# Performance work log

Measured on AMD Instinct MI355X. Metric: run time of the kernel, lower is better.

The kernel has to match this reference:

```python
import jax, jax.numpy as jnp
import numpy as np

N_NODES = 50000


def gcn_conv(x, src, dst, W, b, num_nodes):
    """PyG GCNConv: y = D^{-1/2} (A + I) D^{-1/2} (x @ W) + b.
    src/dst already include self-loops."""
    h = x @ W  # [N, F_out]
    deg = jax.ops.segment_sum(jnp.ones_like(dst, dtype=h.dtype), dst,
                              num_segments=num_nodes)  # in-degree incl. self-loop
    dinv = jnp.where(deg > 0, jax.lax.rsqrt(deg), 0.0)
    norm = dinv[src] * dinv[dst]  # [E]
    msgs = h[src] * norm[:, None]  # gather + scale, [E, F_out]
    out = jax.ops.segment_sum(msgs, dst, num_segments=num_nodes)
    return out + b


def setup_inputs() -> dict:
    key = jax.random.key(0)
    k1, k2, k3, k4 = jax.random.split(key, 4)
    latent, hidden, out_ch = 64, 128, 64
    n_edges = 800000
    z = jax.random.normal(k1, (N_NODES, latent), dtype=jnp.float32)
    edge_index = jax.random.randint(k2, (2, n_edges), 0, N_NODES, dtype=jnp.int64)
    # Glorot-style scaled weights
    W1 = jax.random.normal(k3, (latent, hidden), dtype=jnp.float32) * (1.0 / np.sqrt(latent))
    b1 = jnp.zeros((hidden,), dtype=jnp.float32)
    W2 = jax.random.normal(k4, (hidden, out_ch), dtype=jnp.float32) * (1.0 / np.sqrt(hidden))
    b2 = jnp.zeros((out_ch,), dtype=jnp.float32)
    return {"z": z, "edge_index": edge_index, "W1": W1, "b1": b1, "W2": W2, "b2": b2}


def reference(z, edge_index, W1, b1, W2, b2):
    num_nodes = z.shape[0]
    loops = jnp.arange(num_nodes, dtype=edge_index.dtype)
    src = jnp.concatenate([edge_index[0], loops])  # add self-loops
    dst = jnp.concatenate([edge_index[1], loops])
    x = gcn_conv(z, src, dst, W1, b1, num_nodes)
    x = jax.nn.relu(x)
    x = gcn_conv(x, src, dst, W2, b2, num_nodes)
    x = jax.nn.relu(x)
    return x
```

## Files before the change

### kernel.cpp

```cpp
#include <hip/hip_runtime.h>
#include <hip/hip_fp16.h>

static inline size_t align256(size_t x){ return (x + 255) & ~(size_t)255; }

#define CAP 64
#define NPART 8

__device__ __forceinline__ int detect_is64(const unsigned* __restrict__ e){
  unsigned v = e[2 * (threadIdx.x & 63) + 1];
  return (__ballot(v != 0u) == 0ull) ? 1 : 0;
}

__device__ __forceinline__ int load_idx(const void* edges, long i, int is64){
  return is64 ? (int)((const long long*)edges)[i] : ((const int*)edges)[i];
}

__global__ __launch_bounds__(256) void pack_kernel(const void* __restrict__ edges, int E,
                                                   unsigned* __restrict__ pe,
                                                   int* __restrict__ cnt, int N){
  const int is64 = detect_is64((const unsigned*)edges);
  const int t0 = blockIdx.x * 256 + threadIdx.x;
  const int stride = gridDim.x * 256;
  for (int i = t0; i < N; i += stride) cnt[i] = 0;
  for (int i = t0; i < E; i += stride){
    const unsigned s = (unsigned)load_idx(edges, i, is64);
    const unsigned d = (unsigned)load_idx(edges, (long)E + i, is64);
    pe[i] = (d << 16) | (s & 0xFFFFu);
  }
}

__global__ __launch_bounds__(256) void build_kernel(const unsigned* __restrict__ pe, int E,
                                                    int* __restrict__ cnt,
                                                    unsigned short* __restrict__ csr,
                                                    int N){
  const int p  = blockIdx.x & (NPART - 1);
  const int q  = blockIdx.x >> 3;
  const int nq = gridDim.x >> 3;
  const int nper = (N + NPART - 1) / NPART;
  const int lo = p * nper;
  const int hi = min(lo + nper, N);
  const int stride = nq * 256;
  for (int i = q * 256 + threadIdx.x; i < E; i += stride){
    const unsigned v = pe[i];
    const int d = (int)(v >> 16);
    if (d < lo || d >= hi) continue;
    const int pos = atomicAdd(&cnt[d], 1);
    if (pos < CAP) csr[((size_t)d << 6) + pos] = (unsigned short)(v & 0xFFFFu);
  }
}

__device__ __forceinline__ void h8_acc(uint4 r, float* a){
  const __half2* h = (const __half2*)&r;
  #pragma unroll
  for (int k = 0; k < 4; ++k){
    const float2 f = __half22float2(h[k]);
    a[2*k]     += f.x;
    a[2*k + 1] += f.y;
  }
}

__device__ __forceinline__ void gather8(const uint4* __restrict__ H,
                                        const unsigned short* __restrict__ row,
                                        int deg, int j, float* a){
  int e = 0;
  #pragma unroll 1
  for (; e + 4 <= deg; e += 4){
    const ushort4 rr = *(const ushort4*)(row + e);
    const uint4 v0 = H[(size_t)rr.x * 8 + j];
    const uint4 v1 = H[(size_t)rr.y * 8 + j];
    const uint4 v2 = H[(size_t)rr.z * 8 + j];
    const uint4 v3 = H[(size_t)rr.w * 8 + j];
    h8_acc(v0, a); h8_acc(v1, a); h8_acc(v2, a); h8_acc(v3, a);
  }
  #pragma unroll 1
  for (; e < deg; ++e) h8_acc(H[(size_t)row[e] * 8 + j], a);
}

__global__ __launch_bounds__(256) void prep_kernel(const float4* __restrict__ z,
                                                   uint4* __restrict__ zh,
                                                   const int* __restrict__ cnt,
                                                   float* __restrict__ dinv, int N){
  const int idx = blockIdx.x * 256 + threadIdx.x;
  const int node = idx >> 3;
  if (node >= N) return;
  const int j = idx & 7;
  const float di = rsqrtf((float)(cnt[node] + 1));
  if (j == 0) dinv[node] = di;
  const float4 v0 = z[(size_t)node * 16 + j * 2];
  const float4 v1 = z[(size_t)node * 16 + j * 2 + 1];
  const __half2 a0 = __float22half2_rn(make_float2(di * v0.x, di * v0.y));
  const __half2 a1 = __float22half2_rn(make_float2(di * v0.z, di * v0.w));
  const __half2 a2 = __float22half2_rn(make_float2(di * v1.x, di * v1.y));
  const __half2 a3 = __float22half2_rn(make_float2(di * v1.z, di * v1.w));
  uint4 r;
  r.x = *(const unsigned*)&a0; r.y = *(const unsigned*)&a1;
  r.z = *(const unsigned*)&a2; r.w = *(const unsigned*)&a3;
  zh[idx] = r;
}

#define X1LD 132
__global__ __launch_bounds__(512) void fused1_kernel(const uint4* __restrict__ zh,
                                                     const unsigned short* __restrict__ csr,
                                                     const int* __restrict__ cnt,
                                                     const float* __restrict__ dinv,
                                                     const float* __restrict__ W1,
                                                     const float* __restrict__ b1,
                                                     const float* __restrict__ W2,
                                                     __half* __restrict__ h2, int N){
  __shared__ unsigned short wl[64 * 128];
  __shared__ float rows[64 * 64];
  __shared__ unsigned short x1t[64 * X1LD];
  const int t = threadIdx.x;

  {
    const float4* Wg = (const float4*)W1;
    #pragma unroll
    for (int c = 0; c < 4; ++c){
      const int gi = t + c * 512;
      const float4 v = Wg[gi];
      const __half2 h0 = __float22half2_rn(make_float2(v.x, v.y));
      const __half2 h1 = __float22half2_rn(make_float2(v.z, v.w));
      uint2 r; r.x = *(const unsigned*)&h0; r.y = *(const unsigned*)&h1;
      *(uint2*)&wl[gi * 4] = r;
    }
  }

  const int local = t >> 3;
  const int j = t & 7;
  const int node = blockIdx.x * 64 + local;
  float a[8] = {0.f, 0.f, 0.f, 0.f, 0.f, 0.f, 0.f, 0.f};
  if (node < N){
    h8_acc(zh[(size_t)node * 8 + j], a);
    const int deg = min(cnt[node], CAP);
    gather8(zh, csr + ((size_t)node << 6), deg, j, a);
    const float di = dinv[node];
    #pragma unroll
    for (int k = 0; k < 8; ++k) a[k] *= di;
  }
  float4* rp = (float4*)&rows[t * 8];
  rp[0] = make_float4(a[0], a[1], a[2], a[3]);
  rp[1] = make_float4(a[4], a[5], a[6], a[7]);
  __syncthreads();

  const int jc = t & 127;
  const int g = t >> 7;
  {
    const float bv = b1[jc];
    float accv[16];
    #pragma unroll
    for (int n = 0; n < 16; ++n) accv[n] = bv;

    #pragma unroll 2
    for (int k4 = 0; k4 < 16; ++k4){
      const float w0 = __half2float(*(const __half*)&wl[(4 * k4 + 0) * 128 + jc]);
      const float w1 = __half2float(*(const __half*)&wl[(4 * k4 + 1) * 128 + jc]);
      const float w2 = __half2float(*(const __half*)&wl[(4 * k4 + 2) * 128 + jc]);
      const float w3 = __half2float(*(const __half*)&wl[(4 * k4 + 3) * 128 + jc]);
      #pragma unroll
      for (int n = 0; n < 16; ++n){
        const float4 r = ((const float4*)rows)[(g * 16 + n) * 16 + k4];
        accv[n] = fmaf(r.x, w0, accv[n]);
        accv[n] = fmaf(r.y, w1, accv[n]);
        accv[n] = fmaf(r.z, w2, accv[n]);
        accv[n] = fmaf(r.w, w3, accv[n]);
      }
    }
    #pragma unroll
    for (int n = 0; n < 16; ++n){
      const __half hv = __float2half(fmaxf(accv[n], 0.0f));
      x1t[(g * 16 + n) * X1LD + jc] = *(const unsigned short*)&hv;
    }
  }
  __syncthreads();

  {
    const float4* Wg = (const float4*)W2;
    #pragma unroll
    for (int c = 0; c < 4; ++c){
      const int gi = t + c * 512;
      const float4 v = Wg[gi];
      const __half2 h0 = __float22half2_rn(make_float2(v.x, v.y));
      const __half2 h1 = __float22half2_rn(make_float2(v.z, v.w));
      uint2 r; r.x = *(const unsigned*)&h0; r.y = *(const unsigned*)&h1;
      *(uint2*)&wl[gi * 4] = r;
    }
  }
  __syncthreads();

  const int cg = t & 15;
  const int ng = t >> 4;
  const int n0 = ng * 2, n1 = n0 + 1;
  float acc0[4] = {0.f,0.f,0.f,0.f}, acc1[4] = {0.f,0.f,0.f,0.f};
  #pragma unroll 4
  for (int k4 = 0; k4 < 32; ++k4){
    const int k = k4 * 4;
    const uint2 xa = *(const uint2*)&x1t[n0 * X1LD + k];
    const uint2 xb = *(const uint2*)&x1t[n1 * X1LD + k];
    float xf0[4], xf1[4];
    {
      const float2 p0 = __half22float2(*(const __half2*)&xa.x);
      const float2 p1 = __half22float2(*(const __half2*)&xa.y);
      xf0[0]=p0.x; xf0[1]=p0.y; xf0[2]=p1.x; xf0[3]=p1.y;
      const float2 q0 = __half22float2(*(const __half2*)&xb.x);
      const float2 q1 = __half22float2(*(const __half2*)&xb.y);
      xf1[0]=q0.x; xf1[1]=q0.y; xf1[2]=q1.x; xf1[3]=q1.y;
    }
    #pragma unroll
    for (int dk = 0; dk < 4; ++dk){
      const uint2 wv = *(const uint2*)&wl[(k + dk) * 64 + cg * 4];
      const float2 w01 = __half22float2(*(const __half2*)&wv.x);
      const float2 w23 = __half22float2(*(const __half2*)&wv.y);
      acc0[0] = fmaf(xf0[dk], w01.x, acc0[0]);
      acc0[1] = fmaf(xf0[dk], w01.y, acc0[1]);
      acc0[2] = fmaf(xf0[dk], w23.x, acc0[2]);
      acc0[3] = fmaf(xf0[dk], w23.y, acc0[3]);
      acc1[0] = fmaf(xf1[dk], w01.x, acc1[0]);
      acc1[1] = fmaf(xf1[dk], w01.y, acc1[1]);
      acc1[2] = fmaf(xf1[dk], w23.x, acc1[2]);
      acc1[3] = fmaf(xf1[dk], w23.y, acc1[3]);
    }
  }
  const int gn0 = blockIdx.x * 64 + n0;
  const int gn1 = gn0 + 1;
  if (gn0 < N){
    const float d0 = dinv[gn0];
    const __half2 h0 = __float22half2_rn(make_float2(acc0[0]*d0, acc0[1]*d0));
    const __half2 h1 = __float22half2_rn(make_float2(acc0[2]*d0, acc0[3]*d0));
    uint2 r; r.x = *(const unsigned*)&h0; r.y = *(const unsigned*)&h1;
    *(uint2*)&h2[(size_t)gn0 * 64 + cg * 4] = r;
  }
  if (gn1 < N){
    const float d1 = dinv[gn1];
    const __half2 h0 = __float22half2_rn(make_float2(acc1[0]*d1, acc1[1]*d1));
    const __half2 h1 = __float22half2_rn(make_float2(acc1[2]*d1, acc1[3]*d1));
    uint2 r; r.x = *(const unsigned*)&h0; r.y = *(const unsigned*)&h1;
    *(uint2*)&h2[(size_t)gn1 * 64 + cg * 4] = r;
  }
}

__global__ __launch_bounds__(256) void agg2_kernel(const uint4* __restrict__ X,
                                                   float4* __restrict__ Y,
                                                   const unsigned short* __restrict__ csr,
                                                   const int* __restrict__ cnt,
                                                   const float* __restrict__ dinv,
                                                   const float4* __restrict__ bias,
                                                   int N){
  const int local = threadIdx.x >> 3;
  const int j = threadIdx.x & 7;
  const int node = blockIdx.x * 32 + local;
  if (node >= N) return;
  float a[8] = {0.f, 0.f, 0.f, 0.f, 0.f, 0.f, 0.f, 0.f};
  h8_acc(X[(size_t)node * 8 + j], a);
  const int deg = min(cnt[node], CAP);
  gather8(X, csr + ((size_t)node << 6), deg, j, a);
  const float di = dinv[node];
  const float4 b0 = bias[j * 2];
  const float4 b1v = bias[j * 2 + 1];
  float4 o0, o1;
  o0.x = fmaxf(fmaf(di, a[0], b0.x), 0.f);
  o0.y = fmaxf(fmaf(di, a[1], b0.y), 0.f);
  o0.z = fmaxf(fmaf(di, a[2], b0.z), 0.f);
  o0.w = fmaxf(fmaf(di, a[3], b0.w), 0.f);
  o1.x = fmaxf(fmaf(di, a[4], b1v.x), 0.f);
  o1.y = fmaxf(fmaf(di, a[5], b1v.y), 0.f);
  o1.z = fmaxf(fmaf(di, a[6], b1v.z), 0.f);
  o1.w = fmaxf(fmaf(di, a[7], b1v.w), 0.f);
  Y[(size_t)node * 16 + j * 2] = o0;
  Y[(size_t)node * 16 + j * 2 + 1] = o1;
}

extern "C" void kernel_launch(void* const* d_in, const int* in_sizes, int n_in,
                              void* d_out, int out_size, void* d_ws, size_t ws_size,
                              hipStream_t stream){
  const float* z  = (const float*)d_in[0];
  const void*  edges = d_in[1];
  const float* W1 = (const float*)d_in[2];
  const float* b1 = (const float*)d_in[3];
  const float* W2 = (const float*)d_in[4];
  const float* b2 = (const float*)d_in[5];
  float* out = (float*)d_out;

  constexpr int F0 = 64;
  const int N = in_sizes[0] / F0;
  const int E = in_sizes[1] / 2;
  (void)n_in; (void)out_size;

  char* p = (char*)d_ws;
  int*            cnt  = (int*)p;            p += align256((size_t)N * 4);
  float*          dinv = (float*)p;          p += align256((size_t)N * 4);
  unsigned short* csr  = (unsigned short*)p; p += align256((size_t)N * CAP * 2);
  unsigned*       pe   = (unsigned*)p;       p += align256((size_t)E * 4);
  __half*         zh   = (__half*)p;         p += align256((size_t)N * F0 * 2);
  __half*         h2   = (__half*)p;         p += align256((size_t)N * F0 * 2);
  (void)ws_size;

  pack_kernel<<<1024, 256, 0, stream>>>(edges, E, pe, cnt, N);
  build_kernel<<<1024, 256, 0, stream>>>(pe, E, cnt, csr, N);
  prep_kernel<<<(N * 8 + 255) / 256, 256, 0, stream>>>(
      (const float4*)z, (uint4*)zh, cnt, dinv, N);

  fused1_kernel<<<(N + 63) / 64, 512, 0, stream>>>(
      (const uint4*)zh, csr, cnt, dinv, W1, b1, W2, h2, N);

  agg2_kernel<<<(N + 31) / 32, 256, 0, stream>>>(
      (const uint4*)h2, (float4*)out, csr, cnt, dinv, (const float4*)b2, N);
}
```

Baseline: 196.3 us.

## Split feature tables into two planes and map blocks to XCD node partitions

Stores the fp16 feature tables as two 32-feature planes, so each gather pass touches a half-width, more cache-resident table. The layer-2 aggregation becomes two launches, one per plane, and layer-1 gathers both planes in sequence. Block indices are remapped so that blocks with the same index mod 8 handle one contiguous node partition, which aims to keep each XCD's L2 working set local. The cost is twice as many gather passes over the CSR rows and an extra kernel launch.

```diff
diff --git a/kernel.cpp b/kernel.cpp
--- a/kernel.cpp
+++ b/kernel.cpp
@@ -10,7 +10,6 @@
   unsigned v = e[2 * (threadIdx.x & 63) + 1];
   return (__ballot(v != 0u) == 0ull) ? 1 : 0;
 }
-
 __device__ __forceinline__ int load_idx(const void* edges, long i, int is64){
   return is64 ? (int)((const long long*)edges)[i] : ((const int*)edges)[i];
 }
@@ -49,68 +48,70 @@
   }
 }
 
-__device__ __forceinline__ void h8_acc(uint4 r, float* a){
-  const __half2* h = (const __half2*)&r;
-  #pragma unroll
-  for (int k = 0; k < 4; ++k){
-    const float2 f = __half22float2(h[k]);
-    a[2*k]     += f.x;
-    a[2*k + 1] += f.y;
-  }
-}
-
-__device__ __forceinline__ void gather8(const uint4* __restrict__ H,
+__device__ __forceinline__ void h4_acc(uint2 r, float* a){
+  const float2 f0 = __half22float2(*(const __half2*)&r.x);
+  const float2 f1 = __half22float2(*(const __half2*)&r.y);
+  a[0] += f0.x; a[1] += f0.y; a[2] += f1.x; a[3] += f1.y;
+}
+
+__device__ __forceinline__ void gather4(const uint2* __restrict__ P,
                                         const unsigned short* __restrict__ row,
                                         int deg, int j, float* a){
   int e = 0;
   #pragma unroll 1
-  for (; e + 4 <= deg; e += 4){
-    const ushort4 rr = *(const ushort4*)(row + e);
-    const uint4 v0 = H[(size_t)rr.x * 8 + j];
-    const uint4 v1 = H[(size_t)rr.y * 8 + j];
-    const uint4 v2 = H[(size_t)rr.z * 8 + j];
-    const uint4 v3 = H[(size_t)rr.w * 8 + j];
-    h8_acc(v0, a); h8_acc(v1, a); h8_acc(v2, a); h8_acc(v3, a);
+  for (; e + 8 <= deg; e += 8){
+    const ushort4 r0 = *(const ushort4*)(row + e);
+    const ushort4 r1 = *(const ushort4*)(row + e + 4);
+    const uint2 v0 = P[(size_t)r0.x * 8 + j];
+    const uint2 v1 = P[(size_t)r0.y * 8 + j];
+    const uint2 v2 = P[(size_t)r0.z * 8 + j];
+    const uint2 v3 = P[(size_t)r0.w * 8 + j];
+    const uint2 v4 = P[(size_t)r1.x * 8 + j];
+    const uint2 v5 = P[(size_t)r1.y * 8 + j];
+    const uint2 v6 = P[(size_t)r1.z * 8 + j];
+    const uint2 v7 = P[(size_t)r1.w * 8 + j];
+    h4_acc(v0, a); h4_acc(v1, a); h4_acc(v2, a); h4_acc(v3, a);
+    h4_acc(v4, a); h4_acc(v5, a); h4_acc(v6, a); h4_acc(v7, a);
   }
   #pragma unroll 1
-  for (; e < deg; ++e) h8_acc(H[(size_t)row[e] * 8 + j], a);
+  for (; e < deg; ++e) h4_acc(P[(size_t)row[e] * 8 + j], a);
 }
 
 __global__ __launch_bounds__(256) void prep_kernel(const float4* __restrict__ z,
-                                                   uint4* __restrict__ zh,
+                                                   uint2* __restrict__ zh,
                                                    const int* __restrict__ cnt,
                                                    float* __restrict__ dinv, int N){
   const int idx = blockIdx.x * 256 + threadIdx.x;
-  const int node = idx >> 3;
+  const int node = idx >> 4;
   if (node >= N) return;
-  const int j = idx & 7;
+  const int sub = idx & 15;
+  const int pl = sub >> 3;
+  const int j = sub & 7;
   const float di = rsqrtf((float)(cnt[node] + 1));
-  if (j == 0) dinv[node] = di;
-  const float4 v0 = z[(size_t)node * 16 + j * 2];
-  const float4 v1 = z[(size_t)node * 16 + j * 2 + 1];
-  const __half2 a0 = __float22half2_rn(make_float2(di * v0.x, di * v0.y));
-  const __half2 a1 = __float22half2_rn(make_float2(di * v0.z, di * v0.w));
-  const __half2 a2 = __float22half2_rn(make_float2(di * v1.x, di * v1.y));
-  const __half2 a3 = __float22half2_rn(make_float2(di * v1.z, di * v1.w));
-  uint4 r;
-  r.x = *(const unsigned*)&a0; r.y = *(const unsigned*)&a1;
-  r.z = *(const unsigned*)&a2; r.w = *(const unsigned*)&a3;
-  zh[idx] = r;
+  if (sub == 0) dinv[node] = di;
+  const float4 v = z[(size_t)node * 16 + pl * 8 + j];
+  const __half2 h0 = __float22half2_rn(make_float2(di * v.x, di * v.y));
+  const __half2 h1 = __float22half2_rn(make_float2(di * v.z, di * v.w));
+  uint2 r; r.x = *(const unsigned*)&h0; r.y = *(const unsigned*)&h1;
+  zh[((size_t)pl * N + node) * 8 + j] = r;
 }
 
 #define X1LD 132
-__global__ __launch_bounds__(512) void fused1_kernel(const uint4* __restrict__ zh,
+__global__ __launch_bounds__(512) void fused1_kernel(const uint2* __restrict__ zh,
                                                      const unsigned short* __restrict__ csr,
                                                      const int* __restrict__ cnt,
                                                      const float* __restrict__ dinv,
                                                      const float* __restrict__ W1,
                                                      const float* __restrict__ b1,
                                                      const float* __restrict__ W2,
-                                                     __half* __restrict__ h2, int N){
+                                                     uint2* __restrict__ h2,
+                                                     int N, int NPER){
   __shared__ unsigned short wl[64 * 128];
   __shared__ float rows[64 * 64];
   __shared__ unsigned short x1t[64 * X1LD];
   const int t = threadIdx.x;
+  const int p = blockIdx.x & (NPART - 1);
+  const int q = blockIdx.x >> 3;
 
   {
     const float4* Wg = (const float4*)W1;
@@ -127,19 +128,27 @@
 
   const int local = t >> 3;
   const int j = t & 7;
-  const int node = blockIdx.x * 64 + local;
-  float a[8] = {0.f, 0.f, 0.f, 0.f, 0.f, 0.f, 0.f, 0.f};
-  if (node < N){
-    h8_acc(zh[(size_t)node * 8 + j], a);
-    const int deg = min(cnt[node], CAP);
-    gather8(zh, csr + ((size_t)node << 6), deg, j, a);
-    const float di = dinv[node];
-    #pragma unroll
-    for (int k = 0; k < 8; ++k) a[k] *= di;
-  }
-  float4* rp = (float4*)&rows[t * 8];
-  rp[0] = make_float4(a[0], a[1], a[2], a[3]);
-  rp[1] = make_float4(a[4], a[5], a[6], a[7]);
+  const int ln = q * 64 + local;
+  const int node = p * NPER + ln;
+  const bool valid = (ln < NPER) && (node < N);
+  float di = 0.f; int deg = 0;
+  const unsigned short* row = csr;
+  if (valid){
+    di = dinv[node];
+    deg = min(cnt[node], CAP);
+    row = csr + ((size_t)node << 6);
+  }
+  #pragma unroll
+  for (int pl = 0; pl < 2; ++pl){
+    float a[4] = {0.f, 0.f, 0.f, 0.f};
+    if (valid){
+      const uint2* P = zh + (size_t)pl * N * 8;
+      h4_acc(P[(size_t)node * 8 + j], a);
+      gather4(P, row, deg, j, a);
+    }
+    *(float4*)&rows[local * 64 + pl * 32 + j * 4] =
+        make_float4(a[0] * di, a[1] * di, a[2] * di, a[3] * di);
+  }
   __syncthreads();
 
   const int jc = t & 127;
@@ -220,53 +229,56 @@
       acc1[3] = fmaf(xf1[dk], w23.y, acc1[3]);
     }
   }
-  const int gn0 = blockIdx.x * 64 + n0;
-  const int gn1 = gn0 + 1;
-  if (gn0 < N){
+  const int pl = cg >> 3;
+  const int u2 = cg & 7;
+  const int ln0 = q * 64 + n0;
+  const int gn0 = p * NPER + ln0;
+  if (ln0 < NPER && gn0 < N){
     const float d0 = dinv[gn0];
     const __half2 h0 = __float22half2_rn(make_float2(acc0[0]*d0, acc0[1]*d0));
     const __half2 h1 = __float22half2_rn(make_float2(acc0[2]*d0, acc0[3]*d0));
     uint2 r; r.x = *(const unsigned*)&h0; r.y = *(const unsigned*)&h1;
-    *(uint2*)&h2[(size_t)gn0 * 64 + cg * 4] = r;
-  }
-  if (gn1 < N){
+    h2[((size_t)pl * N + gn0) * 8 + u2] = r;
+  }
+  const int ln1 = ln0 + 1;
+  const int gn1 = gn0 + 1;
+  if (ln1 < NPER && gn1 < N){
     const float d1 = dinv[gn1];
     const __half2 h0 = __float22half2_rn(make_float2(acc1[0]*d1, acc1[1]*d1));
     const __half2 h1 = __float22half2_rn(make_float2(acc1[2]*d1, acc1[3]*d1));
     uint2 r; r.x = *(const unsigned*)&h0; r.y = *(const unsigned*)&h1;
-    *(uint2*)&h2[(size_t)gn1 * 64 + cg * 4] = r;
-  }
-}
-
-__global__ __launch_bounds__(256) void agg2_kernel(const uint4* __restrict__ X,
+    h2[((size_t)pl * N + gn1) * 8 + u2] = r;
+  }
+}
+
+template<int PL>
+__global__ __launch_bounds__(256) void agg2_kernel(const uint2* __restrict__ h2,
                                                    float4* __restrict__ Y,
                                                    const unsigned short* __restrict__ csr,
                                                    const int* __restrict__ cnt,
                                                    const float* __restrict__ dinv,
                                                    const float4* __restrict__ bias,
-                                                   int N){
+                                                   int N, int NPER){
+  const int p = blockIdx.x & (NPART - 1);
+  const int q = blockIdx.x >> 3;
   const int local = threadIdx.x >> 3;
   const int j = threadIdx.x & 7;
-  const int node = blockIdx.x * 32 + local;
-  if (node >= N) return;
-  float a[8] = {0.f, 0.f, 0.f, 0.f, 0.f, 0.f, 0.f, 0.f};
-  h8_acc(X[(size_t)node * 8 + j], a);
+  const int ln = q * 32 + local;
+  const int node = p * NPER + ln;
+  if (ln >= NPER || node >= N) return;
+  const uint2* P = h2 + (size_t)PL * N * 8;
+  float a[4] = {0.f, 0.f, 0.f, 0.f};
+  h4_acc(P[(size_t)node * 8 + j], a);
   const int deg = min(cnt[node], CAP);
-  gather8(X, csr + ((size_t)node << 6), deg, j, a);
+  gather4(P, csr + ((size_t)node << 6), deg, j, a);
   const float di = dinv[node];
-  const float4 b0 = bias[j * 2];
-  const float4 b1v = bias[j * 2 + 1];
-  float4 o0, o1;
-  o0.x = fmaxf(fmaf(di, a[0], b0.x), 0.f);
-  o0.y = fmaxf(fmaf(di, a[1], b0.y), 0.f);
-  o0.z = fmaxf(fmaf(di, a[2], b0.z), 0.f);
-  o0.w = fmaxf(fmaf(di, a[3], b0.w), 0.f);
-  o1.x = fmaxf(fmaf(di, a[4], b1v.x), 0.f);
-  o1.y = fmaxf(fmaf(di, a[5], b1v.y), 0.f);
-  o1.z = fmaxf(fmaf(di, a[6], b1v.z), 0.f);
-  o1.w = fmaxf(fmaf(di, a[7], b1v.w), 0.f);
-  Y[(size_t)node * 16 + j * 2] = o0;
-  Y[(size_t)node * 16 + j * 2 + 1] = o1;
+  const float4 b = bias[PL * 8 + j];
+  float4 o;
+  o.x = fmaxf(fmaf(di, a[0], b.x), 0.f);
+  o.y = fmaxf(fmaf(di, a[1], b.y), 0.f);
+  o.z = fmaxf(fmaf(di, a[2], b.z), 0.f);
+  o.w = fmaxf(fmaf(di, a[3], b.w), 0.f);
+  Y[(size_t)node * 16 + PL * 8 + j] = o;
 }
 
 extern "C" void kernel_launch(void* const* d_in, const int* in_sizes, int n_in,
@@ -283,6 +295,7 @@
   constexpr int F0 = 64;
   const int N = in_sizes[0] / F0;
   const int E = in_sizes[1] / 2;
+  const int NPER = (N + NPART - 1) / NPART;
   (void)n_in; (void)out_size;
 
   char* p = (char*)d_ws;
@@ -290,18 +303,22 @@
   float*          dinv = (float*)p;          p += align256((size_t)N * 4);
   unsigned short* csr  = (unsigned short*)p; p += align256((size_t)N * CAP * 2);
   unsigned*       pe   = (unsigned*)p;       p += align256((size_t)E * 4);
-  __half*         zh   = (__half*)p;         p += align256((size_t)N * F0 * 2);
-  __half*         h2   = (__half*)p;         p += align256((size_t)N * F0 * 2);
+  uint2*          zh   = (uint2*)p;          p += align256((size_t)N * 16 * 8);
+  uint2*          h2   = (uint2*)p;          p += align256((size_t)N * 16 * 8);
   (void)ws_size;
 
   pack_kernel<<<1024, 256, 0, stream>>>(edges, E, pe, cnt, N);
   build_kernel<<<1024, 256, 0, stream>>>(pe, E, cnt, csr, N);
-  prep_kernel<<<(N * 8 + 255) / 256, 256, 0, stream>>>(
-      (const float4*)z, (uint4*)zh, cnt, dinv, N);
-
-  fused1_kernel<<<(N + 63) / 64, 512, 0, stream>>>(
-      (const uint4*)zh, csr, cnt, dinv, W1, b1, W2, h2, N);
-
-  agg2_kernel<<<(N + 31) / 32, 256, 0, stream>>>(
-      (const uint4*)h2, (float4*)out, csr, cnt, dinv, (const float4*)b2, N);
-}
+  prep_kernel<<<(N * 16 + 255) / 256, 256, 0, stream>>>(
+      (const float4*)z, zh, cnt, dinv, N);
+
+  const int grid_f = NPART * ((NPER + 63) / 64);
+  fused1_kernel<<<grid_f, 512, 0, stream>>>(
+      zh, csr, cnt, dinv, W1, b1, W2, h2, N, NPER);
+
+  const int grid_a = NPART * ((NPER + 31) / 32);
+  agg2_kernel<0><<<grid_a, 256, 0, stream>>>(
+      h2, (float4*)out, csr, cnt, dinv, (const float4*)b2, N, NPER);
+  agg2_kernel<1><<<grid_a, 256, 0, stream>>>(
+      h2, (float4*)out, csr, cnt, dinv, (const float4*)b2, N, NPER);
+}
```

Result: slower. 219.6 us (+11.9%).

## Use packed fp16 dot2 instructions with XOR-swizzled LDS layouts in fused GEMMs

Applied to the files above, without the earlier changes.

Both dense matmuls in the fused kernel now use v_dot2 fp16 instructions (via __builtin_amdgcn_fdot2) on k-paired half2 weights and activations instead of per-element fp32 FMAs with half-to-float conversions. The aggregated rows are stored as fp16 pairs, and shared-memory layouts are XOR-swizzled to avoid bank conflicts. Weights are repacked so each word holds two consecutive k values. This halves LDS footprint and instruction count but rounds the layer-1 aggregated input to fp16, which may cost accuracy.

```diff
diff --git a/kernel.cpp b/kernel.cpp
--- a/kernel.cpp
+++ b/kernel.cpp
@@ -10,9 +10,20 @@
   unsigned v = e[2 * (threadIdx.x & 63) + 1];
   return (__ballot(v != 0u) == 0ull) ? 1 : 0;
 }
-
 __device__ __forceinline__ int load_idx(const void* edges, long i, int is64){
   return is64 ? (int)((const long long*)edges)[i] : ((const int*)edges)[i];
+}
+
+__device__ __forceinline__ float fdot2u(unsigned a, unsigned b, float c){
+#if defined(__has_builtin) && __has_builtin(__builtin_amdgcn_fdot2)
+  typedef _Float16 h2 __attribute__((ext_vector_type(2)));
+  return __builtin_amdgcn_fdot2(__builtin_bit_cast(h2, a),
+                                __builtin_bit_cast(h2, b), c, false);
+#else
+  const float2 fa = __half22float2(*(const __half2*)&a);
+  const float2 fb = __half22float2(*(const __half2*)&b);
+  return fmaf(fa.y, fb.y, fmaf(fa.x, fb.x, c));
+#endif
 }
 
 __global__ __launch_bounds__(256) void pack_kernel(const void* __restrict__ edges, int E,
@@ -98,7 +109,6 @@
   zh[idx] = r;
 }
 
-#define X1LD 132
 __global__ __launch_bounds__(512) void fused1_kernel(const uint4* __restrict__ zh,
                                                      const unsigned short* __restrict__ csr,
                                                      const int* __restrict__ cnt,
@@ -107,21 +117,20 @@
                                                      const float* __restrict__ b1,
                                                      const float* __restrict__ W2,
                                                      __half* __restrict__ h2, int N){
-  __shared__ unsigned short wl[64 * 128];
-  __shared__ float rows[64 * 64];
-  __shared__ unsigned short x1t[64 * X1LD];
+  __shared__ unsigned wl[4096];
+  __shared__ unsigned rows2[2048];
+  __shared__ unsigned x1t[4096];
   const int t = threadIdx.x;
 
   {
-    const float4* Wg = (const float4*)W1;
-    #pragma unroll
-    for (int c = 0; c < 4; ++c){
-      const int gi = t + c * 512;
-      const float4 v = Wg[gi];
-      const __half2 h0 = __float22half2_rn(make_float2(v.x, v.y));
-      const __half2 h1 = __float22half2_rn(make_float2(v.z, v.w));
-      uint2 r; r.x = *(const unsigned*)&h0; r.y = *(const unsigned*)&h1;
-      *(uint2*)&wl[gi * 4] = r;
+    #pragma unroll
+    for (int c = 0; c < 8; ++c){
+      const int idx = t + c * 512;
+      const int k2 = idx >> 7, jc = idx & 127;
+      const float w0 = W1[(2 * k2) * 128 + jc];
+      const float w1 = W1[(2 * k2 + 1) * 128 + jc];
+      const __half2 hh = __float22half2_rn(make_float2(w0, w1));
+      wl[idx] = *(const unsigned*)&hh;
     }
   }
 
@@ -129,17 +138,19 @@
   const int j = t & 7;
   const int node = blockIdx.x * 64 + local;
   float a[8] = {0.f, 0.f, 0.f, 0.f, 0.f, 0.f, 0.f, 0.f};
+  float di = 0.f;
   if (node < N){
+    di = dinv[node];
     h8_acc(zh[(size_t)node * 8 + j], a);
     const int deg = min(cnt[node], CAP);
     gather8(zh, csr + ((size_t)node << 6), deg, j, a);
-    const float di = dinv[node];
-    #pragma unroll
-    for (int k = 0; k < 8; ++k) a[k] *= di;
-  }
-  float4* rp = (float4*)&rows[t * 8];
-  rp[0] = make_float4(a[0], a[1], a[2], a[3]);
-  rp[1] = make_float4(a[4], a[5], a[6], a[7]);
+  }
+  #pragma unroll
+  for (int m = 0; m < 4; ++m){
+    const __half2 hh = __float22half2_rn(make_float2(a[2*m] * di, a[2*m+1] * di));
+    const int k2 = (j * 4 + m) ^ (local & 31);
+    rows2[local * 32 + k2] = *(const unsigned*)&hh;
+  }
   __syncthreads();
 
   const int jc = t & 127;
@@ -150,39 +161,35 @@
     #pragma unroll
     for (int n = 0; n < 16; ++n) accv[n] = bv;
 
-    #pragma unroll 2
-    for (int k4 = 0; k4 < 16; ++k4){
-      const float w0 = __half2float(*(const __half*)&wl[(4 * k4 + 0) * 128 + jc]);
-      const float w1 = __half2float(*(const __half*)&wl[(4 * k4 + 1) * 128 + jc]);
-      const float w2 = __half2float(*(const __half*)&wl[(4 * k4 + 2) * 128 + jc]);
-      const float w3 = __half2float(*(const __half*)&wl[(4 * k4 + 3) * 128 + jc]);
+    #pragma unroll 4
+    for (int k2 = 0; k2 < 32; ++k2){
+      const unsigned w = wl[k2 * 128 + jc];
       #pragma unroll
       for (int n = 0; n < 16; ++n){
-        const float4 r = ((const float4*)rows)[(g * 16 + n) * 16 + k4];
-        accv[n] = fmaf(r.x, w0, accv[n]);
-        accv[n] = fmaf(r.y, w1, accv[n]);
-        accv[n] = fmaf(r.z, w2, accv[n]);
-        accv[n] = fmaf(r.w, w3, accv[n]);
+        const int nn = g * 16 + n;
+        accv[n] = fdot2u(rows2[nn * 32 + (k2 ^ (nn & 31))], w, accv[n]);
       }
     }
+    unsigned short* x1h = (unsigned short*)x1t;
     #pragma unroll
     for (int n = 0; n < 16; ++n){
+      const int nn = g * 16 + n;
       const __half hv = __float2half(fmaxf(accv[n], 0.0f));
-      x1t[(g * 16 + n) * X1LD + jc] = *(const unsigned short*)&hv;
+      const int u = nn * 64 + ((jc >> 1) ^ ((nn & 7) << 3));
+      x1h[u * 2 + (jc & 1)] = *(const unsigned short*)&hv;
     }
   }
   __syncthreads();
 
   {
-    const float4* Wg = (const float4*)W2;
-    #pragma unroll
-    for (int c = 0; c < 4; ++c){
-      const int gi = t + c * 512;
-      const float4 v = Wg[gi];
-      const __half2 h0 = __float22half2_rn(make_float2(v.x, v.y));
-      const __half2 h1 = __float22half2_rn(make_float2(v.z, v.w));
-      uint2 r; r.x = *(const unsigned*)&h0; r.y = *(const unsigned*)&h1;
-      *(uint2*)&wl[gi * 4] = r;
+    #pragma unroll
+    for (int c = 0; c < 8; ++c){
+      const int idx = t + c * 512;
+      const int k2 = idx >> 6, jc2 = idx & 63;
+      const float w0 = W2[(2 * k2) * 64 + jc2];
+      const float w1 = W2[(2 * k2 + 1) * 64 + jc2];
+      const __half2 hh = __float22half2_rn(make_float2(w0, w1));
+      wl[idx] = *(const unsigned*)&hh;
     }
   }
   __syncthreads();
@@ -192,33 +199,18 @@
   const int n0 = ng * 2, n1 = n0 + 1;
   float acc0[4] = {0.f,0.f,0.f,0.f}, acc1[4] = {0.f,0.f,0.f,0.f};
   #pragma unroll 4
-  for (int k4 = 0; k4 < 32; ++k4){
-    const int k = k4 * 4;
-    const uint2 xa = *(const uint2*)&x1t[n0 * X1LD + k];
-    const uint2 xb = *(const uint2*)&x1t[n1 * X1LD + k];
-    float xf0[4], xf1[4];
-    {
-      const float2 p0 = __half22float2(*(const __half2*)&xa.x);
-      const float2 p1 = __half22float2(*(const __half2*)&xa.y);
-      xf0[0]=p0.x; xf0[1]=p0.y; xf0[2]=p1.x; xf0[3]=p1.y;
-      const float2 q0 = __half22float2(*(const __half2*)&xb.x);
-      const float2 q1 = __half22float2(*(const __half2*)&xb.y);
-      xf1[0]=q0.x; xf1[1]=q0.y; xf1[2]=q1.x; xf1[3]=q1.y;
-    }
-    #pragma unroll
-    for (int dk = 0; dk < 4; ++dk){
-      const uint2 wv = *(const uint2*)&wl[(k + dk) * 64 + cg * 4];
-      const float2 w01 = __half22float2(*(const __half2*)&wv.x);
-      const float2 w23 = __half22float2(*(const __half2*)&wv.y);
-      acc0[0] = fmaf(xf0[dk], w01.x, acc0[0]);
-      acc0[1] = fmaf(xf0[dk], w01.y, acc0[1]);
-      acc0[2] = fmaf(xf0[dk], w23.x, acc0[2]);
-      acc0[3] = fmaf(xf0[dk], w23.y, acc0[3]);
-      acc1[0] = fmaf(xf1[dk], w01.x, acc1[0]);
-      acc1[1] = fmaf(xf1[dk], w01.y, acc1[1]);
-      acc1[2] = fmaf(xf1[dk], w23.x, acc1[2]);
-      acc1[3] = fmaf(xf1[dk], w23.y, acc1[3]);
-    }
+  for (int k2 = 0; k2 < 64; ++k2){
+    const unsigned xa = x1t[n0 * 64 + (k2 ^ ((n0 & 7) << 3))];
+    const unsigned xb = x1t[n1 * 64 + (k2 ^ ((n1 & 7) << 3))];
+    const uint4 wv = *(const uint4*)&wl[k2 * 64 + cg * 4];
+    acc0[0] = fdot2u(xa, wv.x, acc0[0]);
+    acc0[1] = fdot2u(xa, wv.y, acc0[1]);
+    acc0[2] = fdot2u(xa, wv.z, acc0[2]);
+    acc0[3] = fdot2u(xa, wv.w, acc0[3]);
+    acc1[0] = fdot2u(xb, wv.x, acc1[0]);
+    acc1[1] = fdot2u(xb, wv.y, acc1[1]);
+    acc1[2] = fdot2u(xb, wv.z, acc1[2]);
+    acc1[3] = fdot2u(xb, wv.w, acc1[3]);
   }
   const int gn0 = blockIdx.x * 64 + n0;
   const int gn1 = gn0 + 1;
```

Result: faster. 191.4 us (-2.5%).
